# Optimization experiments

Hardware: AMD Instinct MI355X
Metric: run time of the kernel (lower is better)

## Reference

```python
import jax, jax.numpy as jnp
import numpy as np

B, N, D, H = 4, 2048, 512, 8
HD = D // H
SCALE = D ** (-0.5)  # module uses embed_dim**-0.5, not head_dim**-0.5


def setup_inputs() -> dict:
    key = jax.random.key(0)
    k1, k2, k3, k4 = jax.random.split(key, 4)
    x = jax.random.normal(k1, (B, N, D), dtype=jnp.float32)
    # qkv: Linear(D, 3D, bias=False); store as [D, 3D] (x @ W_qkv)
    w_qkv = jax.random.normal(k2, (D, 3 * D), dtype=jnp.float32) * (D ** -0.5)
    # out_proj: Linear(D, D) with bias
    w_out = jax.random.normal(k3, (D, D), dtype=jnp.float32) * (D ** -0.5)
    b_out = jax.random.normal(k4, (D,), dtype=jnp.float32) * 0.01
    return {"x": x, "w_qkv": w_qkv, "w_out": w_out, "b_out": b_out}


def reference(x, w_qkv, w_out, b_out):
    # qkv projection -> [B, N, 3, H, HD] -> split
    qkv = (x @ w_qkv).reshape(B, N, 3, H, HD)
    q = qkv[:, :, 0].transpose(0, 2, 1, 3)  # [B, H, N, HD]
    k = qkv[:, :, 1].transpose(0, 2, 1, 3)
    v = qkv[:, :, 2].transpose(0, 2, 1, 3)
    attn = jnp.einsum("bhqd,bhkd->bhqk", q, k) * SCALE  # [B, H, N, N]
    attn = jax.nn.softmax(attn, axis=-1)
    out = jnp.einsum("bhqk,bhkd->bhqd", attn, v)  # [B, H, N, HD]
    out = out.transpose(0, 2, 1, 3).reshape(B, N, D)
    return out @ w_out + b_out
```

## Files before the change

### kernel.cpp

```cpp
#include <hip/hip_runtime.h>

typedef __attribute__((ext_vector_type(4))) float f32x4;
typedef __attribute__((ext_vector_type(16))) float f32x16;
typedef __attribute__((ext_vector_type(8))) short short8;

#define DEV static __device__ __forceinline__

DEV unsigned short f2bf(float f) {
  union { float f; unsigned u; } x; x.f = f;
  unsigned r = x.u + 0x7fffu + ((x.u >> 16) & 1u);
  return (unsigned short)(r >> 16);
}

DEV float bf2f(unsigned short u) {
  union { unsigned u; float f; } x; x.u = ((unsigned)u) << 16;
  return x.f;
}

DEV f32x4 mfma16(short8 a, short8 b, f32x4 c) {
  return __builtin_amdgcn_mfma_f32_16x16x32_bf16(a, b, c, 0, 0, 0);
}

DEV f32x16 mfma32(short8 a, short8 b, f32x16 c) {
  return __builtin_amdgcn_mfma_f32_32x32x16_bf16(a, b, c, 0, 0, 0);
}

DEV void gload16(const void* g, void* l) {
  __builtin_amdgcn_global_load_lds(
      (const __attribute__((address_space(1))) void*)g,
      (__attribute__((address_space(3))) void*)l, 16, 0, 0);
}

DEV float exp2f_fast(float x) {
  float r;
  asm("v_exp_f32 %0, %1" : "=v"(r) : "v"(x));
  return r;
}

DEV unsigned cvtpk(float lo, float hi) {
  unsigned r;
  asm("v_cvt_pk_bf16_f32 %0, %1, %2" : "=v"(r) : "v"(lo), "v"(hi));
  return r;
}

DEV short8 mk8(unsigned w0, unsigned w1, unsigned w2, unsigned w3) {
  union { unsigned u[4]; short8 s; } x;
  x.u[0] = w0; x.u[1] = w1; x.u[2] = w2; x.u[3] = w3;
  return x.s;
}

DEV int swzrow(int r) { return (((r & 7) ^ ((r >> 3) & 7)) << 3); }

__global__ __launch_bounds__(256) void k_prep(
    const float* __restrict__ x, unsigned short* __restrict__ xb,
    const float* __restrict__ wq, unsigned short* __restrict__ wqT,
    const float* __restrict__ wo, unsigned short* __restrict__ woT) {
  __shared__ unsigned short T[64 * 72];
  const int blk = blockIdx.x;
  const int t = threadIdx.x;
  if (blk < 2048) {
    size_t i = (size_t)blk * 256 + t;
    const f32x4* p = (const f32x4*)(x + i * 8);
    f32x4 a = p[0], b = p[1];
    short8 r;
    r[0] = f2bf(a[0]); r[1] = f2bf(a[1]); r[2] = f2bf(a[2]); r[3] = f2bf(a[3]);
    r[4] = f2bf(b[0]); r[5] = f2bf(b[1]); r[6] = f2bf(b[2]); r[7] = f2bf(b[3]);
    *(short8*)(xb + i * 8) = r;
    return;
  }
  const float* in;
  unsigned short* out;
  int C, bx, by;
  const int R = 512;
  if (blk < 2240) {
    in = wq; out = wqT; C = 1536;
    int bb = blk - 2048; bx = bb % 24; by = bb / 24;
  } else {
    in = wo; out = woT; C = 512;
    int bb = blk - 2240; bx = bb & 7; by = bb >> 3;
  }
  int r0 = by * 64, c0 = bx * 64;
  int rr = t >> 2, seg = t & 3;
  const float* p = in + (size_t)(r0 + rr) * C + c0 + seg * 16;
#pragma unroll
  for (int q = 0; q < 4; ++q) {
    f32x4 v = *(const f32x4*)(p + q * 4);
#pragma unroll
    for (int e = 0; e < 4; ++e) T[rr * 72 + seg * 16 + q * 4 + e] = f2bf(v[e]);
  }
  __syncthreads();
  short8 o0, o1;
#pragma unroll
  for (int e = 0; e < 8; ++e) o0[e] = (short)T[(seg * 16 + e) * 72 + rr];
#pragma unroll
  for (int e = 0; e < 8; ++e) o1[e] = (short)T[(seg * 16 + 8 + e) * 72 + rr];
  unsigned short* q2 = out + (size_t)(c0 + rr) * R + r0 + seg * 16;
  *(short8*)q2 = o0;
  *(short8*)(q2 + 8) = o1;
}

__global__ __launch_bounds__(256) void k_build_vt(const unsigned short* __restrict__ qkv,
                                                  unsigned short* __restrict__ vt) {
  __shared__ unsigned short T[64 * 72];
  int n0 = blockIdx.x * 64;
  int bh = blockIdx.y;
  int b = bh >> 3, h = bh & 7;
  int t = threadIdx.x;
  int rr = t >> 2, seg = t & 3;
  const unsigned short* p =
      qkv + (size_t)(b * 2048 + n0 + rr) * 1536 + 1024 + h * 64 + seg * 16;
  *(short8*)&T[rr * 72 + seg * 16] = *(const short8*)p;
  *(short8*)&T[rr * 72 + seg * 16 + 8] = *(const short8*)(p + 8);
  __syncthreads();
  short8 o0, o1;
#pragma unroll
  for (int e = 0; e < 8; ++e) o0[e] = (short)T[(seg * 16 + e) * 72 + rr];
#pragma unroll
  for (int e = 0; e < 8; ++e) o1[e] = (short)T[(seg * 16 + 8 + e) * 72 + rr];
  unsigned short* q2 = vt + (size_t)(bh * 64 + rr) * 2048 + n0 + seg * 16;
  *(short8*)q2 = o0;
  *(short8*)(q2 + 8) = o1;
}

template <bool F32OUT>
__global__ __launch_bounds__(256) void k_gemm_bt(
    const unsigned short* __restrict__ A, const unsigned short* __restrict__ Bt,
    void* __restrict__ Cp, const float* __restrict__ bias, int M, int N, int K) {
  __shared__ unsigned short Asm[128 * 64];
  __shared__ unsigned short Bsm[128 * 64];
  const int tid = threadIdx.x;
  const int lane = tid & 63, w = tid >> 6;
  const int wr = w >> 1, wc = w & 1;
  const int nbx = gridDim.x;
  const int cpx = (nbx * gridDim.y) >> 3;
  const int lin = blockIdx.y * nbx + blockIdx.x;
  const int swz = (lin & 7) * cpx + (lin >> 3);
  const int bm = (swz / nbx) * 128, bn = (swz % nbx) * 128;
  const int l15 = lane & 15, l4 = lane >> 4;
  f32x4 acc[4][4] = {};
  for (int k0 = 0; k0 < K; k0 += 64) {
    __syncthreads();
#pragma unroll
    for (int j = 0; j < 4; ++j) {
      int c = j * 256 + tid;
      gload16(A + (size_t)(bm + (c >> 3)) * K + k0 + ((c & 7) << 3),
              Asm + (size_t)(j * 256 + w * 64) * 8);
    }
#pragma unroll
    for (int j = 0; j < 4; ++j) {
      int c = j * 256 + tid;
      gload16(Bt + (size_t)(bn + (c >> 3)) * K + k0 + ((c & 7) << 3),
              Bsm + (size_t)(j * 256 + w * 64) * 8);
    }
    __syncthreads();
#pragma unroll
    for (int kc = 0; kc < 2; ++kc) {
      short8 av[4], bv[4];
#pragma unroll
      for (int i = 0; i < 4; ++i)
        av[i] = *(const short8*)&Asm[(wr * 64 + i * 16 + l15) * 64 + kc * 32 + l4 * 8];
#pragma unroll
      for (int j = 0; j < 4; ++j)
        bv[j] = *(const short8*)&Bsm[(wc * 64 + j * 16 + l15) * 64 + kc * 32 + l4 * 8];
#pragma unroll
      for (int i = 0; i < 4; ++i)
#pragma unroll
        for (int j = 0; j < 4; ++j)
          acc[i][j] = mfma16(av[i], bv[j], acc[i][j]);
    }
  }
#pragma unroll
  for (int i = 0; i < 4; ++i) {
#pragma unroll
    for (int j = 0; j < 4; ++j) {
      int col = bn + wc * 64 + j * 16 + l15;
      float bb = 0.f;
      if constexpr (F32OUT) bb = bias[col];
#pragma unroll
      for (int v = 0; v < 4; ++v) {
        int row = bm + wr * 64 + i * 16 + l4 * 4 + v;
        if constexpr (F32OUT) {
          ((float*)Cp)[(size_t)row * N + col] = acc[i][j][v] + bb;
        } else {
          ((unsigned short*)Cp)[(size_t)row * N + col] = f2bf(acc[i][j][v]);
        }
      }
    }
  }
}

__global__ __launch_bounds__(512, 4) void k_attn5(const unsigned short* __restrict__ qkv,
                                                  const unsigned short* __restrict__ vtg,
                                                  unsigned short* __restrict__ O) {
  __shared__ unsigned short smem[16896];
  unsigned short* Ks0 = smem;
  unsigned short* Ks1 = smem + 4096;
  unsigned short* Vs0 = smem + 8192;
  unsigned short* Vs1 = smem + 12288;
  const int tid = threadIdx.x;
  const int lane = tid & 63, w = tid >> 6;
  const int qg = w & 3, half = w >> 2;
  const int l31 = lane & 31, hi = lane >> 5;
  const int bh = blockIdx.y, b = bh >> 3, h = bh & 7;
  const int q0 = blockIdx.x * 128 + qg * 32;
  const float CL = 0.044194173824159216f * 1.4426950408889634f;

  short8 qf[4];
  {
    const unsigned short* qp = qkv + (size_t)(b * 2048 + q0 + l31) * 1536 + h * 64;
#pragma unroll
    for (int ks = 0; ks < 4; ++ks) {
      short8 raw = *(const short8*)(qp + ks * 16 + hi * 8);
      short8 f;
#pragma unroll
      for (int e = 0; e < 8; ++e)
        f[e] = (short)f2bf(bf2f((unsigned short)raw[e]) * CL);
      qf[ks] = f;
    }
  }

  const int sr = tid >> 3, seg = tid & 7;
  const unsigned short* kg = qkv + (size_t)b * 2048 * 1536 + 512 + h * 64 + seg * 8;
  const unsigned short* vg = vtg + (size_t)bh * 64 * 2048 + seg * 8;
  const int so = sr * 64 + ((seg * 8) ^ swzrow(sr));

  *(short8*)&Ks0[so] = *(const short8*)(kg + (size_t)sr * 1536);
  *(short8*)&Vs0[so] = *(const short8*)(vg + (size_t)sr * 2048);
  __syncthreads();

  const int kxor = swzrow(half * 32 + l31);
  const int v0xor = swzrow(l31);
  const int v1xor = swzrow(32 + l31);
  const int krow = (half * 32 + l31) * 64;

  f32x16 oacc0 = {}, oacc1 = {};
  float m_run = 0.f, l_run = 0.f;
  unsigned short* kcur = Ks0; unsigned short* knxt = Ks1;
  unsigned short* vcur = Vs0; unsigned short* vnxt = Vs1;

  for (int t = 0; t < 32; ++t) {
    short8 pk, pv;
    if (t < 31) {
      int kv = (t + 1) * 64;
      pk = *(const short8*)(kg + (size_t)(kv + sr) * 1536);
      pv = *(const short8*)(vg + (size_t)sr * 2048 + kv);
    }

    f32x16 st = {};
    __builtin_amdgcn_s_setprio(1);
#pragma unroll
    for (int ks = 0; ks < 4; ++ks) {
      int col = ks * 16 + hi * 8;
      short8 kf = *(const short8*)&kcur[krow + (col ^ kxor)];
      st = mfma32(kf, qf[ks], st);
    }
    __builtin_amdgcn_s_setprio(0);

    float tm[8];
#pragma unroll
    for (int r = 0; r < 8; ++r) tm[r] = fmaxf(st[r], st[r + 8]);
    float pm = fmaxf(fmaxf(fmaxf(tm[0], tm[1]), fmaxf(tm[2], tm[3])),
                     fmaxf(fmaxf(tm[4], tm[5]), fmaxf(tm[6], tm[7])));
    pm = fmaxf(pm, __shfl_xor(pm, 32));

    if (!__all(pm <= m_run + 11.5f)) {
      float mn = fmaxf(m_run, pm);
      float al = exp2f_fast(m_run - mn);
#pragma unroll
      for (int r = 0; r < 16; ++r) {
        int qd = (r & 3) + 8 * (r >> 2) + 4 * hi;
        float a = __shfl(al, qd);
        oacc0[r] *= a;
        oacc1[r] *= a;
      }
      l_run *= al;
      m_run = mn;
    }

    float p[16];
    float la = 0.f, lb = 0.f;
#pragma unroll
    for (int r = 0; r < 8; ++r) { p[r] = exp2f_fast(st[r] - m_run); la += p[r]; }
#pragma unroll
    for (int r = 8; r < 16; ++r) { p[r] = exp2f_fast(st[r] - m_run); lb += p[r]; }
    float lsum = la + lb;
    short8 pa[2];
#pragma unroll
    for (int g = 0; g < 2; ++g) {
      unsigned pkA0 = cvtpk(p[8 * g + 0], p[8 * g + 1]);
      unsigned pkA1 = cvtpk(p[8 * g + 2], p[8 * g + 3]);
      unsigned pkB0 = cvtpk(p[8 * g + 4], p[8 * g + 5]);
      unsigned pkB1 = cvtpk(p[8 * g + 6], p[8 * g + 7]);
      unsigned tA0 = __shfl_xor(pkA0, 32), tA1 = __shfl_xor(pkA1, 32);
      unsigned tB0 = __shfl_xor(pkB0, 32), tB1 = __shfl_xor(pkB1, 32);
      unsigned w0 = hi ? tB0 : pkA0;
      unsigned w1 = hi ? tB1 : pkA1;
      unsigned w2 = hi ? pkB0 : tA0;
      unsigned w3 = hi ? pkB1 : tA1;
      pa[g] = mk8(w0, w1, w2, w3);
    }
    lsum += __shfl_xor(lsum, 32);
    l_run += lsum;

    __builtin_amdgcn_s_setprio(1);
#pragma unroll
    for (int ks = 0; ks < 2; ++ks) {
      int col = (half * 2 + ks) * 16 + hi * 8;
      short8 vf0 = *(const short8*)&vcur[l31 * 64 + (col ^ v0xor)];
      short8 vf1 = *(const short8*)&vcur[(32 + l31) * 64 + (col ^ v1xor)];
      oacc0 = mfma32(pa[ks], vf0, oacc0);
      oacc1 = mfma32(pa[ks], vf1, oacc1);
    }
    __builtin_amdgcn_s_setprio(0);

    if (t < 31) {
      *(short8*)&knxt[so] = pk;
      *(short8*)&vnxt[so] = pv;
    }
    __syncthreads();
    { unsigned short* tp = kcur; kcur = knxt; knxt = tp; }
    { unsigned short* tp = vcur; vcur = vnxt; vnxt = tp; }
  }

  float* Opart = (float*)smem;
  float* mlbuf = (float*)(smem + 16384);
  if (half == 1) {
    float* op = Opart + qg * 2048;
#pragma unroll
    for (int r = 0; r < 16; ++r) {
      int qd = (r & 3) + 8 * (r >> 2) + 4 * hi;
      op[qd * 64 + l31] = oacc0[r];
      op[qd * 64 + 32 + l31] = oacc1[r];
    }
    if (hi == 0) {
      mlbuf[qg * 64 + l31] = m_run;
      mlbuf[qg * 64 + 32 + l31] = l_run;
    }
  }
  __syncthreads();
  if (half == 0) {
    float mb = mlbuf[qg * 64 + l31];
    float lb2 = mlbuf[qg * 64 + 32 + l31];
    float mmax = fmaxf(m_run, mb);
    float sa = exp2f_fast(m_run - mmax);
    float sb = exp2f_fast(mb - mmax);
    float dI = 1.0f / (l_run * sa + lb2 * sb);
    float fA = sa * dI, fB = sb * dI;
    const float* op = Opart + qg * 2048;
#pragma unroll
    for (int r = 0; r < 16; ++r) {
      int qd = (r & 3) + 8 * (r >> 2) + 4 * hi;
      float fa = __shfl(fA, qd), fb = __shfl(fB, qd);
      float o0 = oacc0[r] * fa + op[qd * 64 + l31] * fb;
      float o1 = oacc1[r] * fa + op[qd * 64 + 32 + l31] * fb;
      size_t row = (size_t)(b * 2048 + q0 + qd) * 512 + h * 64;
      O[row + l31] = f2bf(o0);
      O[row + 32 + l31] = f2bf(o1);
    }
  }
}

extern "C" void kernel_launch(void* const* d_in, const int* in_sizes, int n_in,
                              void* d_out, int out_size, void* d_ws, size_t ws_size,
                              hipStream_t stream) {
  const float* x = (const float*)d_in[0];
  const float* w_qkv = (const float*)d_in[1];
  const float* w_out = (const float*)d_in[2];
  const float* b_out = (const float*)d_in[3];
  float* out = (float*)d_out;
  char* ws = (char*)d_ws;

  unsigned short* xb    = (unsigned short*)(ws + 0);
  unsigned short* wqkvT = (unsigned short*)(ws + 8388608);
  unsigned short* woutT = (unsigned short*)(ws + 9961472);
  unsigned short* qkvb  = (unsigned short*)(ws + 10485760);
  unsigned short* vtb   = (unsigned short*)(ws + 35651584);
  unsigned short* Ob    = (unsigned short*)(ws + 44040192);

  k_prep<<<2304, 256, 0, stream>>>(x, xb, w_qkv, wqkvT, w_out, woutT);
  k_gemm_bt<false><<<dim3(12, 64), 256, 0, stream>>>(xb, wqkvT, (void*)qkvb, nullptr,
                                                     8192, 1536, 512);
  k_build_vt<<<dim3(32, 32), 256, 0, stream>>>(qkvb, vtb);
  k_attn5<<<dim3(16, 32), 512, 0, stream>>>(qkvb, vtb, Ob);
  k_gemm_bt<true><<<dim3(4, 64), 256, 0, stream>>>(Ob, woutT, (void*)out, b_out,
                                                   8192, 512, 512);
}
```

Baseline: 175.4 us.

## Fuse V transpose into QKV GEMM epilogue and narrow out-proj tiles

The QKV projection GEMM now writes the V-column tiles directly in transposed layout through an LDS staging buffer, which removes the separate k_build_vt kernel launch and its extra read and write of V. The output projection uses 128x64 tiles, doubling the grid to 512 blocks so more CUs have work. In exchange the GEMM uses more shared memory (34 KB per block) and has a divergent epilogue. The V blocks no longer write V into qkvb, so this is only correct if attention reads V solely from vtb.

```diff
diff --git a/kernel.cpp b/kernel.cpp
--- a/kernel.cpp
+++ b/kernel.cpp
@@ -99,35 +99,16 @@
   *(short8*)(q2 + 8) = o1;
 }
 
-__global__ __launch_bounds__(256) void k_build_vt(const unsigned short* __restrict__ qkv,
-                                                  unsigned short* __restrict__ vt) {
-  __shared__ unsigned short T[64 * 72];
-  int n0 = blockIdx.x * 64;
-  int bh = blockIdx.y;
-  int b = bh >> 3, h = bh & 7;
-  int t = threadIdx.x;
-  int rr = t >> 2, seg = t & 3;
-  const unsigned short* p =
-      qkv + (size_t)(b * 2048 + n0 + rr) * 1536 + 1024 + h * 64 + seg * 16;
-  *(short8*)&T[rr * 72 + seg * 16] = *(const short8*)p;
-  *(short8*)&T[rr * 72 + seg * 16 + 8] = *(const short8*)(p + 8);
-  __syncthreads();
-  short8 o0, o1;
-#pragma unroll
-  for (int e = 0; e < 8; ++e) o0[e] = (short)T[(seg * 16 + e) * 72 + rr];
-#pragma unroll
-  for (int e = 0; e < 8; ++e) o1[e] = (short)T[(seg * 16 + 8 + e) * 72 + rr];
-  unsigned short* q2 = vt + (size_t)(bh * 64 + rr) * 2048 + n0 + seg * 16;
-  *(short8*)q2 = o0;
-  *(short8*)(q2 + 8) = o1;
-}
-
-template <bool F32OUT>
+template <bool F32OUT, int NT, bool WVT>
 __global__ __launch_bounds__(256) void k_gemm_bt(
     const unsigned short* __restrict__ A, const unsigned short* __restrict__ Bt,
-    void* __restrict__ Cp, const float* __restrict__ bias, int M, int N, int K) {
-  __shared__ unsigned short Asm[128 * 64];
-  __shared__ unsigned short Bsm[128 * 64];
+    void* __restrict__ Cp, const float* __restrict__ bias,
+    unsigned short* __restrict__ vt, int M, int N, int K) {
+  constexpr int NJ = NT / 32;
+  constexpr int SHSZ = WVT ? (128 * 136) : (8192 + NT * 64);
+  __shared__ unsigned short SH[SHSZ];
+  unsigned short* Asm = SH;
+  unsigned short* Bsm = SH + 8192;
   const int tid = threadIdx.x;
   const int lane = tid & 63, w = tid >> 6;
   const int wr = w >> 1, wc = w & 1;
@@ -135,9 +116,9 @@
   const int cpx = (nbx * gridDim.y) >> 3;
   const int lin = blockIdx.y * nbx + blockIdx.x;
   const int swz = (lin & 7) * cpx + (lin >> 3);
-  const int bm = (swz / nbx) * 128, bn = (swz % nbx) * 128;
+  const int bm = (swz / nbx) * 128, bn = (swz % nbx) * NT;
   const int l15 = lane & 15, l4 = lane >> 4;
-  f32x4 acc[4][4] = {};
+  f32x4 acc[4][NJ] = {};
   for (int k0 = 0; k0 < K; k0 += 64) {
     __syncthreads();
 #pragma unroll
@@ -147,7 +128,7 @@
               Asm + (size_t)(j * 256 + w * 64) * 8);
     }
 #pragma unroll
-    for (int j = 0; j < 4; ++j) {
+    for (int j = 0; j < NJ; ++j) {
       int c = j * 256 + tid;
       gload16(Bt + (size_t)(bn + (c >> 3)) * K + k0 + ((c & 7) << 3),
               Bsm + (size_t)(j * 256 + w * 64) * 8);
@@ -155,25 +136,49 @@
     __syncthreads();
 #pragma unroll
     for (int kc = 0; kc < 2; ++kc) {
-      short8 av[4], bv[4];
+      short8 av[4], bv[NJ];
 #pragma unroll
       for (int i = 0; i < 4; ++i)
         av[i] = *(const short8*)&Asm[(wr * 64 + i * 16 + l15) * 64 + kc * 32 + l4 * 8];
 #pragma unroll
-      for (int j = 0; j < 4; ++j)
-        bv[j] = *(const short8*)&Bsm[(wc * 64 + j * 16 + l15) * 64 + kc * 32 + l4 * 8];
+      for (int j = 0; j < NJ; ++j)
+        bv[j] = *(const short8*)&Bsm[(wc * (NT / 2) + j * 16 + l15) * 64 + kc * 32 + l4 * 8];
 #pragma unroll
       for (int i = 0; i < 4; ++i)
 #pragma unroll
-        for (int j = 0; j < 4; ++j)
+        for (int j = 0; j < NJ; ++j)
           acc[i][j] = mfma16(av[i], bv[j], acc[i][j]);
     }
   }
+  if (WVT && bn >= 1024) {
+    __syncthreads();
+#pragma unroll
+    for (int i = 0; i < 4; ++i)
+#pragma unroll
+      for (int j = 0; j < NJ; ++j) {
+        int colL = wc * (NT / 2) + j * 16 + l15;
+#pragma unroll
+        for (int v = 0; v < 4; ++v)
+          SH[colL * 136 + wr * 64 + i * 16 + l4 * 4 + v] = f2bf(acc[i][j][v]);
+      }
+    __syncthreads();
+    const int vtrow = tid >> 1, half2 = tid & 1;
+    const int b2 = bm >> 11, npos0 = bm & 2047;
+    const int h = ((bn - 1024) >> 6) + (vtrow >> 6);
+    const int hd = vtrow & 63;
+    unsigned short* dst =
+        vt + ((size_t)(b2 * 8 + h) * 64 + hd) * 2048 + npos0 + half2 * 64;
+    const unsigned short* srcT = SH + vtrow * 136 + half2 * 64;
+#pragma unroll
+    for (int e = 0; e < 8; ++e)
+      *(short8*)(dst + e * 8) = *(const short8*)(srcT + e * 8);
+    return;
+  }
 #pragma unroll
   for (int i = 0; i < 4; ++i) {
 #pragma unroll
-    for (int j = 0; j < 4; ++j) {
-      int col = bn + wc * 64 + j * 16 + l15;
+    for (int j = 0; j < NJ; ++j) {
+      int col = bn + wc * (NT / 2) + j * 16 + l15;
       float bb = 0.f;
       if constexpr (F32OUT) bb = bias[col];
 #pragma unroll
@@ -378,10 +383,9 @@
   unsigned short* Ob    = (unsigned short*)(ws + 44040192);
 
   k_prep<<<2304, 256, 0, stream>>>(x, xb, w_qkv, wqkvT, w_out, woutT);
-  k_gemm_bt<false><<<dim3(12, 64), 256, 0, stream>>>(xb, wqkvT, (void*)qkvb, nullptr,
-                                                     8192, 1536, 512);
-  k_build_vt<<<dim3(32, 32), 256, 0, stream>>>(qkvb, vtb);
+  k_gemm_bt<false, 128, true><<<dim3(12, 64), 256, 0, stream>>>(
+      xb, wqkvT, (void*)qkvb, nullptr, vtb, 8192, 1536, 512);
   k_attn5<<<dim3(16, 32), 512, 0, stream>>>(qkvb, vtb, Ob);
-  k_gemm_bt<true><<<dim3(4, 64), 256, 0, stream>>>(Ob, woutT, (void*)out, b_out,
-                                                   8192, 512, 512);
-}
+  k_gemm_bt<true, 64, false><<<dim3(8, 64), 256, 0, stream>>>(
+      Ob, woutT, (void*)out, b_out, nullptr, 8192, 512, 512);
+}
```

New measurement: 173.4 us. Within noise of the previous version (-1.1%).
